# Performance work log

Measured on AMD Instinct MI355X. Metric: run time of the kernel, lower is better.

The kernel has to match this reference:

```python
import jax, jax.numpy as jnp
import numpy as np

TEMPERATURE = 1.0
EPS = 1e-12  # matches torch F.normalize default eps


def setup_inputs() -> dict:
    key = jax.random.key(0)
    k1, k2 = jax.random.split(key)
    B, N, D = 8, 2048, 768
    final_features = jax.random.normal(k1, (B, N, D), dtype=jnp.float32)
    mid_features = jax.random.normal(k2, (B, N, D), dtype=jnp.float32)
    return {"final_features": final_features, "mid_features": mid_features}


def reference(final_features, mid_features):
    B, N, D = final_features.shape
    dtype = final_features.dtype

    mid = mid_features.astype(jnp.float32)
    # L2-normalize along feature dim (torch F.normalize: x / max(||x||, eps))
    norm = jnp.maximum(jnp.linalg.norm(mid, axis=-1, keepdims=True), EPS)
    mid_n = mid / norm

    # [B, N, N] cosine similarity
    sim = jnp.einsum("bnd,bmd->bnm", mid_n, mid_n)
    # zero out diagonal (add_self_similarity=False): sim * (1 - eye)
    eye = jnp.eye(N, dtype=sim.dtype)
    sim = sim * (1.0 - eye)[None, :, :]

    # confidence = row-wise max of (zeroed-diagonal) similarity
    confidence = jnp.max(sim, axis=-1)  # [B, N]

    # softmax over scaled similarities (diagonal entries are exactly 0, kept in softmax)
    weights = jax.nn.softmax(sim / TEMPERATURE, axis=-1)  # [B, N, N]

    refined = jnp.einsum("bnm,bmd->bnd", weights, final_features.astype(jnp.float32))

    cw = confidence[..., None].astype(dtype)  # [B, N, 1]
    calibrated = cw * refined.astype(dtype) + (1.0 - cw) * final_features
    return calibrated
```

## Files before the change

kernel.cpp:

```cpp
#include <hip/hip_runtime.h>
#include <hip/hip_bf16.h>

static constexpr int BB = 8;
static constexpr int NN = 2048;
static constexpr int DD = 768;

typedef __attribute__((ext_vector_type(8))) __bf16 bf16x8;
typedef __attribute__((ext_vector_type(4))) float f32x4;

__device__ __forceinline__ void gload_lds16(const __hip_bfloat16* g, __hip_bfloat16* l) {
  __builtin_amdgcn_global_load_lds(
      (const __attribute__((address_space(1))) void*)g,
      (__attribute__((address_space(3))) void*)l,
      16, 0, 0);
}

static constexpr int NORM_BLOCKS = (BB * NN) / 4;
static constexpr int TRANS_BLOCKS = BB * (NN / 64) * (DD / 64);
static constexpr int QK_BLOCKS = BB * 136;

__global__ void prep_kernel(const float* __restrict__ mid, __hip_bfloat16* __restrict__ Qn,
                            float* __restrict__ lsum, float* __restrict__ conf,
                            const float* __restrict__ F, __hip_bfloat16* __restrict__ Vt) {
  __shared__ __hip_bfloat16 tile[64][68];
  const int t = threadIdx.x;
  if (blockIdx.x < NORM_BLOCKS) {
    const int wave = t >> 6;
    const int lane = t & 63;
    const size_t row = (size_t)blockIdx.x * 4 + wave;
    if (lane == 0) { lsum[row] = 0.f; conf[row] = 0.f; }
    const float* src = mid + row * DD;

    float4 v[3];
    float ss = 0.f;
#pragma unroll
    for (int j = 0; j < 3; ++j) {
      v[j] = *(const float4*)(src + j * 256 + lane * 4);
      ss += v[j].x * v[j].x + v[j].y * v[j].y + v[j].z * v[j].z + v[j].w * v[j].w;
    }
#pragma unroll
    for (int o = 32; o; o >>= 1) ss += __shfl_xor(ss, o, 64);
    const float inv = 1.0f / fmaxf(sqrtf(ss), 1e-12f);

    __hip_bfloat16* dst = Qn + row * DD;
#pragma unroll
    for (int j = 0; j < 3; ++j) {
      union { ushort4 u; __hip_bfloat16 h[4]; } pk;
      pk.h[0] = __float2bfloat16(v[j].x * inv);
      pk.h[1] = __float2bfloat16(v[j].y * inv);
      pk.h[2] = __float2bfloat16(v[j].z * inv);
      pk.h[3] = __float2bfloat16(v[j].w * inv);
      *(ushort4*)(dst + j * 256 + lane * 4) = pk.u;
    }
  } else {
    const int bid = blockIdx.x - NORM_BLOCKS;
    const int bx = bid % (DD / 64);
    const int rest = bid / (DD / 64);
    const int by = rest & 31;
    const int b = rest >> 5;
    const int n0 = by * 64;
    const int d0 = bx * 64;
    const int tr = t >> 4;
    const int tc = t & 15;
#pragma unroll
    for (int i = 0; i < 4; ++i) {
      const int n = tr + i * 16;
      const float4 v = *(const float4*)(F + ((size_t)b * NN + n0 + n) * DD + d0 + tc * 4);
      union { ushort4 u; __hip_bfloat16 h[4]; } pk;
      pk.h[0] = __float2bfloat16(v.x);
      pk.h[1] = __float2bfloat16(v.y);
      pk.h[2] = __float2bfloat16(v.z);
      pk.h[3] = __float2bfloat16(v.w);
      *(ushort4*)&tile[n][tc * 4] = pk.u;
    }
    __syncthreads();
#pragma unroll
    for (int i = 0; i < 4; ++i) {
      const int dd = tr + i * 16;
      const int n4 = tc * 4;
      union { ushort4 u; __hip_bfloat16 h[4]; } pk;
#pragma unroll
      for (int j = 0; j < 4; ++j) pk.h[j] = tile[n4 + j][dd];
      *(ushort4*)(Vt + ((size_t)b * DD + d0 + dd) * NN + n0 + n4) = pk.u;
    }
  }
}

__global__ __launch_bounds__(256) void gemm_qk_kernel(
    const __hip_bfloat16* __restrict__ Qn,
    __hip_bfloat16* __restrict__ P,
    float* __restrict__ lsum,
    unsigned* __restrict__ conf) {
  __shared__ __hip_bfloat16 smem[4 * 128 * 64];
  const int t = threadIdx.x;

  const int d = blockIdx.x;
  const int b = d & 7;
  int rem = d >> 3;
  int ti, tj;
  if (rem < 120) {
    ti = 0;
    while (rem >= 15 - ti) { rem -= 15 - ti; ++ti; }
    tj = ti + 1 + rem;
  } else {
    ti = tj = rem - 120;
  }
  const int rowBase = ti * 128;
  const int colBase = tj * 128;
  const bool offdiag = (ti != tj);

  const int lane = t & 63;
  const int wave = t >> 6;
  const int wRow = wave >> 1;
  const int wCol = wave & 1;
  const int quad = lane >> 4;
  const int l16 = lane & 15;

  const __hip_bfloat16* Abase = Qn + ((size_t)b * NN + rowBase) * DD;
  const __hip_bfloat16* Bbase = Qn + ((size_t)b * NN + colBase) * DD;

  int srow[4], scol[4], sc8[4];
#pragma unroll
  for (int i = 0; i < 4; ++i) {
    const int c = i * 256 + t;
    srow[i] = c >> 3;
    const int col8 = (c & 7) ^ ((c >> 3) & 7);
    scol[i] = col8 * 8;
    sc8[i] = c * 8;
  }

  f32x4 acc[4][4];
#pragma unroll
  for (int i = 0; i < 4; ++i)
#pragma unroll
    for (int j = 0; j < 4; ++j) acc[i][j] = (f32x4){0.f, 0.f, 0.f, 0.f};

  {
    __hip_bfloat16* As = smem;
    __hip_bfloat16* Bs = smem + 128 * 64;
#pragma unroll
    for (int i = 0; i < 4; ++i) {
      gload_lds16(Abase + (size_t)srow[i] * DD + scol[i], As + sc8[i]);
      gload_lds16(Bbase + (size_t)srow[i] * DD + scol[i], Bs + sc8[i]);
    }
  }

  constexpr int NK = DD / 64;
  for (int kk = 0; kk < NK; ++kk) {
    const int cur = kk & 1;
    __syncthreads();
    if (kk + 1 < NK) {
      __hip_bfloat16* As = smem + (1 - cur) * 2 * 128 * 64;
      __hip_bfloat16* Bs = As + 128 * 64;
      const int k0 = (kk + 1) * 64;
#pragma unroll
      for (int i = 0; i < 4; ++i) {
        gload_lds16(Abase + (size_t)srow[i] * DD + (k0 + scol[i]), As + sc8[i]);
        gload_lds16(Bbase + (size_t)srow[i] * DD + (k0 + scol[i]), Bs + sc8[i]);
      }
    }
    const __hip_bfloat16* As = smem + cur * 2 * 128 * 64;
    const __hip_bfloat16* Bs = As + 128 * 64;
#pragma unroll
    for (int ks = 0; ks < 2; ++ks) {
      bf16x8 af[4], bfr[4];
#pragma unroll
      for (int i = 0; i < 4; ++i) {
        const int rA = wRow * 64 + i * 16 + l16;
        const int rB = wCol * 64 + i * 16 + l16;
        const int pA = (ks * 4 + quad) ^ (rA & 7);
        const int pB = (ks * 4 + quad) ^ (rB & 7);
        af[i]  = *(const bf16x8*)(As + rA * 64 + pA * 8);
        bfr[i] = *(const bf16x8*)(Bs + rB * 64 + pB * 8);
      }
#pragma unroll
      for (int mi = 0; mi < 4; ++mi)
#pragma unroll
        for (int ni = 0; ni < 4; ++ni)
          acc[mi][ni] = __builtin_amdgcn_mfma_f32_16x16x32_bf16(af[mi], bfr[ni], acc[mi][ni], 0, 0, 0);
    }
  }

  __syncthreads();
  __hip_bfloat16* Pt = smem;
  __hip_bfloat16* Mt = smem + 128 * 128;

  float csum[4] = {0.f, 0.f, 0.f, 0.f};
  float cmax[4] = {0.f, 0.f, 0.f, 0.f};

#pragma unroll
  for (int mi = 0; mi < 4; ++mi) {
    const int rbase = wRow * 64 + mi * 16 + quad * 4;
    float rs[4] = {0.f, 0.f, 0.f, 0.f};
    float rm[4] = {0.f, 0.f, 0.f, 0.f};
#pragma unroll
    for (int ni = 0; ni < 4; ++ni) {
      const int colL = wCol * 64 + ni * 16 + l16;
      const int col_g = colBase + colL;
      union { ushort4 u; __hip_bfloat16 h[4]; } pk;
#pragma unroll
      for (int r = 0; r < 4; ++r) {
        const int rowL = rbase + r;
        float s = acc[mi][ni][r];
        if (rowBase + rowL == col_g) s = 0.f;
        const float p = __expf(s);
        rm[r] = fmaxf(rm[r], s);
        rs[r] += p;
        csum[ni] += p;
        cmax[ni] = fmaxf(cmax[ni], s);
        pk.h[r] = __float2bfloat16(p);
        Pt[rowL * 128 + (((colL >> 3) ^ (rowL & 7)) << 3) + (colL & 7)] = pk.h[r];
      }
      if (offdiag) {
        *(ushort4*)(Mt + colL * 128 + (((rbase >> 3) ^ (colL & 7)) << 3) + (rbase & 7)) = pk.u;
      }
    }
#pragma unroll
    for (int r = 0; r < 4; ++r) {
      float ps = rs[r], mx = rm[r];
#pragma unroll
      for (int o = 1; o < 16; o <<= 1) {
        ps += __shfl_xor(ps, o, 64);
        mx = fmaxf(mx, __shfl_xor(mx, o, 64));
      }
      if (l16 == 0) {
        const int row_g = rowBase + rbase + r;
        atomicAdd(lsum + (size_t)b * NN + row_g, ps);
        atomicMax(conf + (size_t)b * NN + row_g, __float_as_uint(mx));
      }
    }
  }

  if (offdiag) {
#pragma unroll
    for (int ni = 0; ni < 4; ++ni) {
      float cs = csum[ni];
      float cm = cmax[ni];
      cs += __shfl_xor(cs, 16, 64); cm = fmaxf(cm, __shfl_xor(cm, 16, 64));
      cs += __shfl_xor(cs, 32, 64); cm = fmaxf(cm, __shfl_xor(cm, 32, 64));
      if (quad == 0) {
        const int col_g = colBase + wCol * 64 + ni * 16 + l16;
        atomicAdd(lsum + (size_t)b * NN + col_g, cs);
        atomicMax(conf + (size_t)b * NN + col_g, __float_as_uint(cm));
      }
    }
  }

  __syncthreads();
  {
    const size_t pBase = ((size_t)b * NN + rowBase) * (size_t)NN + colBase;
#pragma unroll
    for (int i = 0; i < 8; ++i) {
      const int c = i * 256 + t;
      const int row = c >> 4;
      const int ck = c & 15;
      *(uint4*)(P + pBase + (size_t)row * NN + ck * 8) =
          *(const uint4*)(Pt + row * 128 + ((ck ^ (row & 7)) << 3));
    }
  }
  if (offdiag) {
    const size_t pBase = ((size_t)b * NN + colBase) * (size_t)NN + rowBase;
#pragma unroll
    for (int i = 0; i < 8; ++i) {
      const int c = i * 256 + t;
      const int row = c >> 4;
      const int ck = c & 15;
      *(uint4*)(P + pBase + (size_t)row * NN + ck * 8) =
          *(const uint4*)(Mt + row * 128 + ((ck ^ (row & 7)) << 3));
    }
  }
}

__global__ __launch_bounds__(256) void gemm_pv_kernel(
    const __hip_bfloat16* __restrict__ P,
    const __hip_bfloat16* __restrict__ Vt,
    const float* __restrict__ lsum,
    const float* __restrict__ conf,
    const float* __restrict__ F,
    float* __restrict__ Out) {
  __shared__ __hip_bfloat16 smem[2 * (128 * 64 + 192 * 64)];

  const int d = blockIdx.x;
  const int work = (d & 7) * 64 + (d >> 3);
  const int b = work >> 6;
  const int w6 = work & 63;
  const int colBase = (w6 & 3) * 192;
  const int rowBase = (w6 >> 2) * 128;

  const int t = threadIdx.x;
  const int lane = t & 63;
  const int wave = t >> 6;
  const int wRow = wave >> 1;
  const int wCol = wave & 1;
  const int quad = lane >> 4;
  const int l16 = lane & 15;

  const __hip_bfloat16* Abase = P + (size_t)b * NN * NN + (size_t)rowBase * NN;
  const __hip_bfloat16* Bbase = Vt + (size_t)b * DD * NN + (size_t)colBase * NN;

  int srowA[4], scolA[4], sc8A[4];
#pragma unroll
  for (int i = 0; i < 4; ++i) {
    const int c = i * 256 + t;
    srowA[i] = c >> 3;
    scolA[i] = ((c & 7) ^ ((c >> 3) & 7)) * 8;
    sc8A[i] = c * 8;
  }
  int srowB[6], scolB[6], sc8B[6];
#pragma unroll
  for (int i = 0; i < 6; ++i) {
    const int c = i * 256 + t;
    srowB[i] = c >> 3;
    scolB[i] = ((c & 7) ^ ((c >> 3) & 7)) * 8;
    sc8B[i] = c * 8;
  }

  f32x4 acc[4][6];
#pragma unroll
  for (int i = 0; i < 4; ++i)
#pragma unroll
    for (int j = 0; j < 6; ++j) acc[i][j] = (f32x4){0.f, 0.f, 0.f, 0.f};

  constexpr int ABUF = 128 * 64;
  constexpr int BUFSTRIDE = 128 * 64 + 192 * 64;

  {
    __hip_bfloat16* As = smem;
    __hip_bfloat16* Bs = smem + ABUF;
#pragma unroll
    for (int i = 0; i < 4; ++i)
      gload_lds16(Abase + (size_t)srowA[i] * NN + scolA[i], As + sc8A[i]);
#pragma unroll
    for (int i = 0; i < 6; ++i)
      gload_lds16(Bbase + (size_t)srowB[i] * NN + scolB[i], Bs + sc8B[i]);
  }

  constexpr int NK = NN / 64;
  for (int kk = 0; kk < NK; ++kk) {
    const int cur = kk & 1;
    __syncthreads();
    if (kk + 1 < NK) {
      __hip_bfloat16* As = smem + (1 - cur) * BUFSTRIDE;
      __hip_bfloat16* Bs = As + ABUF;
      const int k0 = (kk + 1) * 64;
#pragma unroll
      for (int i = 0; i < 4; ++i)
        gload_lds16(Abase + (size_t)srowA[i] * NN + (k0 + scolA[i]), As + sc8A[i]);
#pragma unroll
      for (int i = 0; i < 6; ++i)
        gload_lds16(Bbase + (size_t)srowB[i] * NN + (k0 + scolB[i]), Bs + sc8B[i]);
    }
    const __hip_bfloat16* As = smem + cur * BUFSTRIDE;
    const __hip_bfloat16* Bs = As + ABUF;
#pragma unroll
    for (int ks = 0; ks < 2; ++ks) {
      bf16x8 af[4], bfr[6];
#pragma unroll
      for (int i = 0; i < 4; ++i) {
        const int rA = wRow * 64 + i * 16 + l16;
        const int pA = (ks * 4 + quad) ^ (rA & 7);
        af[i] = *(const bf16x8*)(As + rA * 64 + pA * 8);
      }
#pragma unroll
      for (int i = 0; i < 6; ++i) {
        const int rB = wCol * 96 + i * 16 + l16;
        const int pB = (ks * 4 + quad) ^ (rB & 7);
        bfr[i] = *(const bf16x8*)(Bs + rB * 64 + pB * 8);
      }
#pragma unroll
      for (int mi = 0; mi < 4; ++mi)
#pragma unroll
        for (int ni = 0; ni < 6; ++ni)
          acc[mi][ni] = __builtin_amdgcn_mfma_f32_16x16x32_bf16(af[mi], bfr[ni], acc[mi][ni], 0, 0, 0);
    }
  }

#pragma unroll
  for (int mi = 0; mi < 4; ++mi) {
#pragma unroll
    for (int r = 0; r < 4; ++r) {
      const int row_g = rowBase + wRow * 64 + mi * 16 + quad * 4 + r;
      const float li = lsum[(size_t)b * NN + row_g];
      const float cw = conf[(size_t)b * NN + row_g];
      const float inv = 1.0f / li;
      const float* frow = F + ((size_t)b * NN + row_g) * DD;
      float* orow = Out + ((size_t)b * NN + row_g) * DD;
#pragma unroll
      for (int ni = 0; ni < 6; ++ni) {
        const int col_g = colBase + wCol * 96 + ni * 16 + l16;
        const float o = acc[mi][ni][r] * inv;
        orow[col_g] = cw * o + (1.f - cw) * frow[col_g];
      }
    }
  }
}

extern "C" void kernel_launch(void* const* d_in, const int* in_sizes, int n_in,
                              void* d_out, int out_size, void* d_ws, size_t ws_size,
                              hipStream_t stream) {
  const float* F = (const float*)d_in[0];
  const float* M = (const float*)d_in[1];
  float* Out = (float*)d_out;

  char* ws = (char*)d_ws;
  __hip_bfloat16* Qn = (__hip_bfloat16*)(ws);
  __hip_bfloat16* Vt = (__hip_bfloat16*)(ws + 25165824);
  __hip_bfloat16* P  = (__hip_bfloat16*)(ws + 50331648);
  float* lsum        = (float*)(ws + 117440512);
  float* conf        = (float*)(ws + 117506048);

  prep_kernel<<<NORM_BLOCKS + TRANS_BLOCKS, 256, 0, stream>>>(M, Qn, lsum, conf, F, Vt);
  gemm_qk_kernel<<<QK_BLOCKS, 256, 0, stream>>>(Qn, P, lsum, (unsigned*)conf);
  gemm_pv_kernel<<<512, 256, 0, stream>>>(P, Vt, lsum, conf, F, Out);
}
```

Baseline: 254.9 us.

## Single-buffer QK LDS tiles and write P directly to global for occupancy

Halves the QK kernel's shared memory by dropping the double-buffered prefetch, so the next k-tile load now waits behind a barrier after compute. It also removes the LDS staging of the P tile and its transpose and writes bf16 values straight to global memory with scalar and 8-byte stores. A launch-bounds hint of 3 blocks per SM is added to raise occupancy. The trade is lost load/compute overlap within a block and poorly coalesced, narrow global stores, which matter because P is a large bf16 array.

```diff
diff --git a/kernel.cpp b/kernel.cpp
--- a/kernel.cpp
+++ b/kernel.cpp
@@ -86,12 +86,12 @@
   }
 }
 
-__global__ __launch_bounds__(256) void gemm_qk_kernel(
+__global__ __launch_bounds__(256, 3) void gemm_qk_kernel(
     const __hip_bfloat16* __restrict__ Qn,
     __hip_bfloat16* __restrict__ P,
     float* __restrict__ lsum,
     unsigned* __restrict__ conf) {
-  __shared__ __hip_bfloat16 smem[4 * 128 * 64];
+  __shared__ __hip_bfloat16 smem[2 * 128 * 64];
   const int t = threadIdx.x;
 
   const int d = blockIdx.x;
@@ -135,32 +135,18 @@
 #pragma unroll
     for (int j = 0; j < 4; ++j) acc[i][j] = (f32x4){0.f, 0.f, 0.f, 0.f};
 
-  {
-    __hip_bfloat16* As = smem;
-    __hip_bfloat16* Bs = smem + 128 * 64;
-#pragma unroll
-    for (int i = 0; i < 4; ++i) {
-      gload_lds16(Abase + (size_t)srow[i] * DD + scol[i], As + sc8[i]);
-      gload_lds16(Bbase + (size_t)srow[i] * DD + scol[i], Bs + sc8[i]);
-    }
+  __hip_bfloat16* As = smem;
+  __hip_bfloat16* Bs = smem + 128 * 64;
+
+#pragma unroll
+  for (int i = 0; i < 4; ++i) {
+    gload_lds16(Abase + (size_t)srow[i] * DD + scol[i], As + sc8[i]);
+    gload_lds16(Bbase + (size_t)srow[i] * DD + scol[i], Bs + sc8[i]);
   }
 
   constexpr int NK = DD / 64;
   for (int kk = 0; kk < NK; ++kk) {
-    const int cur = kk & 1;
     __syncthreads();
-    if (kk + 1 < NK) {
-      __hip_bfloat16* As = smem + (1 - cur) * 2 * 128 * 64;
-      __hip_bfloat16* Bs = As + 128 * 64;
-      const int k0 = (kk + 1) * 64;
-#pragma unroll
-      for (int i = 0; i < 4; ++i) {
-        gload_lds16(Abase + (size_t)srow[i] * DD + (k0 + scol[i]), As + sc8[i]);
-        gload_lds16(Bbase + (size_t)srow[i] * DD + (k0 + scol[i]), Bs + sc8[i]);
-      }
-    }
-    const __hip_bfloat16* As = smem + cur * 2 * 128 * 64;
-    const __hip_bfloat16* Bs = As + 128 * 64;
 #pragma unroll
     for (int ks = 0; ks < 2; ++ks) {
       bf16x8 af[4], bfr[4];
@@ -179,11 +165,19 @@
         for (int ni = 0; ni < 4; ++ni)
           acc[mi][ni] = __builtin_amdgcn_mfma_f32_16x16x32_bf16(af[mi], bfr[ni], acc[mi][ni], 0, 0, 0);
     }
-  }
-
-  __syncthreads();
-  __hip_bfloat16* Pt = smem;
-  __hip_bfloat16* Mt = smem + 128 * 128;
+    if (kk + 1 < NK) {
+      __syncthreads();
+      const int k0 = (kk + 1) * 64;
+#pragma unroll
+      for (int i = 0; i < 4; ++i) {
+        gload_lds16(Abase + (size_t)srow[i] * DD + (k0 + scol[i]), As + sc8[i]);
+        gload_lds16(Bbase + (size_t)srow[i] * DD + (k0 + scol[i]), Bs + sc8[i]);
+      }
+    }
+  }
+
+  __hip_bfloat16* Pdir = P + ((size_t)b * NN + rowBase) * NN + colBase;
+  __hip_bfloat16* Pmir = P + ((size_t)b * NN + colBase) * NN + rowBase;
 
   float csum[4] = {0.f, 0.f, 0.f, 0.f};
   float cmax[4] = {0.f, 0.f, 0.f, 0.f};
@@ -209,10 +203,10 @@
         csum[ni] += p;
         cmax[ni] = fmaxf(cmax[ni], s);
         pk.h[r] = __float2bfloat16(p);
-        Pt[rowL * 128 + (((colL >> 3) ^ (rowL & 7)) << 3) + (colL & 7)] = pk.h[r];
+        Pdir[(size_t)rowL * NN + colL] = pk.h[r];
       }
       if (offdiag) {
-        *(ushort4*)(Mt + colL * 128 + (((rbase >> 3) ^ (colL & 7)) << 3) + (rbase & 7)) = pk.u;
+        *(ushort4*)(Pmir + (size_t)colL * NN + rbase) = pk.u;
       }
     }
 #pragma unroll
@@ -245,30 +239,6 @@
       }
     }
   }
-
-  __syncthreads();
-  {
-    const size_t pBase = ((size_t)b * NN + rowBase) * (size_t)NN + colBase;
-#pragma unroll
-    for (int i = 0; i < 8; ++i) {
-      const int c = i * 256 + t;
-      const int row = c >> 4;
-      const int ck = c & 15;
-      *(uint4*)(P + pBase + (size_t)row * NN + ck * 8) =
-          *(const uint4*)(Pt + row * 128 + ((ck ^ (row & 7)) << 3));
-    }
-  }
-  if (offdiag) {
-    const size_t pBase = ((size_t)b * NN + colBase) * (size_t)NN + rowBase;
-#pragma unroll
-    for (int i = 0; i < 8; ++i) {
-      const int c = i * 256 + t;
-      const int row = c >> 4;
-      const int ck = c & 15;
-      *(uint4*)(P + pBase + (size_t)row * NN + ck * 8) =
-          *(const uint4*)(Mt + row * 128 + ((ck ^ (row & 7)) << 3));
-    }
-  }
 }
 
 __global__ __launch_bounds__(256) void gemm_pv_kernel(
```

Result: no change. 251.1 us (-1.5%).
